# Kernel tuning notes

Measured on AMD Instinct MI355X. Metric: run time of the kernel, lower is better.

The kernel has to match this reference:

```python
import jax, jax.numpy as jnp
import numpy as np

MD = 4  # max displacement -> (2*MD+1)**2 = 81 output channels

def setup_inputs() -> dict:
    key = jax.random.key(0)
    k1, k2 = jax.random.split(key)
    B, C, H, W = 4, 128, 128, 256
    t1 = jax.random.normal(k1, (B, C, H, W), dtype=jnp.float32)
    t2 = jax.random.normal(k2, (B, C, H, W), dtype=jnp.float32)
    return {"t1": t1, "t2": t2}

def reference(t1, t2):
    # PWC-Net correlation: for each displacement (dy,dx) in [-MD,MD]^2,
    # corr[b, d, y, x] = mean_c t1[b,c,y,x] * t2[b,c,y+dy,x+dx]
    B, C, H, W = t1.shape
    t2p = jnp.pad(t2, ((0, 0), (0, 0), (MD, MD), (MD, MD)))
    outs = []
    for dy in range(2 * MD + 1):
        for dx in range(2 * MD + 1):
            shifted = t2p[:, :, dy:dy + H, dx:dx + W]  # (B,C,H,W)
            outs.append(jnp.mean(t1 * shifted, axis=1))  # (B,H,W)
    return jnp.stack(outs, axis=1)  # (B, 81, H, W)
```

## Files before the change

kernel.cpp:

```cpp
#include <hip/hip_runtime.h>

#define MD   4
#define B_   4
#define C_   128
#define H_   128
#define W_   256
#define ND   9
#define NW   9
#define XPT  4

typedef float float4v __attribute__((ext_vector_type(4)));

__global__ __launch_bounds__(NW * 64, 5)
void corr_kernel(const float* __restrict__ t1,
                 const float* __restrict__ t2,
                 float* __restrict__ out) {
    const int tid  = threadIdx.x;
    const int lane = tid & 63;
    const int w    = tid >> 6;
    const int bid  = blockIdx.x;
    const int swz  = (bid & 7) * 64 + (bid >> 3);
    const int y    = swz & (H_ - 1);
    const int b    = swz >> 7;
    const int x0   = lane * XPT;
    const int yy   = y + w - MD;
    const float scale = 1.0f / (float)C_;

    if (yy < 0 || yy >= H_) {
        float4v z = {0.f, 0.f, 0.f, 0.f};
        #pragma unroll
        for (int dx = 0; dx < ND; ++dx) {
            const size_t oidx =
                (((size_t)(b * ND * ND) + w * ND + dx) * H_ + y) * W_ + x0;
            *(float4v*)&out[oidx] = z;
        }
        return;
    }

    float acc[ND][XPT];
    #pragma unroll
    for (int dx = 0; dx < ND; ++dx)
        #pragma unroll
        for (int j = 0; j < XPT; ++j) acc[dx][j] = 0.0f;

    const float* p1 = t1 + (((size_t)(b * C_)) * H_ + y ) * W_ + x0;
    const float* p2 = t2 + (((size_t)(b * C_)) * H_ + yy) * W_ + x0;
    const size_t chstr = (size_t)H_ * W_;

    const bool lm = (lane == 0);
    const bool rm = (lane == 63);

    #pragma unroll 2
    for (int c = 0; c < C_; ++c) {
        const float4v a = *(const float4v*)(p1 + (size_t)c * chstr);
        const float4v v = *(const float4v*)(p2 + (size_t)c * chstr);

        float win[XPT + 2 * MD];
        #pragma unroll
        for (int k = 0; k < 4; ++k) {
            const float up = __shfl_up(v[k], 1);
            const float dn = __shfl_down(v[k], 1);
            win[k]     = lm ? 0.0f : up;
            win[4 + k] = v[k];
            win[8 + k] = rm ? 0.0f : dn;
        }

        #pragma unroll
        for (int dx = 0; dx < ND; ++dx)
            #pragma unroll
            for (int j = 0; j < XPT; ++j)
                acc[dx][j] = fmaf(a[j], win[dx + j], acc[dx][j]);
    }

    #pragma unroll
    for (int dx = 0; dx < ND; ++dx) {
        float4v o;
        #pragma unroll
        for (int j = 0; j < XPT; ++j) o[j] = acc[dx][j] * scale;
        const size_t oidx =
            (((size_t)(b * ND * ND) + w * ND + dx) * H_ + y) * W_ + x0;
        *(float4v*)&out[oidx] = o;
    }
}

extern "C" void kernel_launch(void* const* d_in, const int* in_sizes, int n_in,
                              void* d_out, int out_size, void* d_ws, size_t ws_size,
                              hipStream_t stream) {
    const float* t1 = (const float*)d_in[0];
    const float* t2 = (const float*)d_in[1];
    float* out      = (float*)d_out;
    corr_kernel<<<dim3(B_ * H_), NW * 64, 0, stream>>>(t1, t2, out);
}
```

Measured before the change: 77.21 us.

## Process two output rows per block with eight columns per thread

Each wavefront now splits into two half-waves covering two adjacent output rows, and each thread computes eight x positions instead of four. This halves the grid and gives each thread more FMAs per shuffled neighbour value. Out-of-range rows no longer return early. They clamp their load row and zero the scale factor, so those waves do full, redundant work instead of skipping it. Register pressure rises (72 accumulators) and the occupancy hint drops from 5 to 3.

```diff
diff --git a/kernel.cpp b/kernel.cpp
--- a/kernel.cpp
+++ b/kernel.cpp
@@ -7,11 +7,11 @@
 #define W_   256
 #define ND   9
 #define NW   9
-#define XPT  4
+#define XPT  8
 
 typedef float float4v __attribute__((ext_vector_type(4)));
 
-__global__ __launch_bounds__(NW * 64, 5)
+__global__ __launch_bounds__(NW * 64, 3)
 void corr_kernel(const float* __restrict__ t1,
                  const float* __restrict__ t2,
                  float* __restrict__ out) {
@@ -19,23 +19,20 @@
     const int lane = tid & 63;
     const int w    = tid >> 6;
     const int bid  = blockIdx.x;
-    const int swz  = (bid & 7) * 64 + (bid >> 3);
-    const int y    = swz & (H_ - 1);
-    const int b    = swz >> 7;
-    const int x0   = lane * XPT;
-    const int yy   = y + w - MD;
-    const float scale = 1.0f / (float)C_;
-
-    if (yy < 0 || yy >= H_) {
-        float4v z = {0.f, 0.f, 0.f, 0.f};
-        #pragma unroll
-        for (int dx = 0; dx < ND; ++dx) {
-            const size_t oidx =
-                (((size_t)(b * ND * ND) + w * ND + dx) * H_ + y) * W_ + x0;
-            *(float4v*)&out[oidx] = z;
-        }
-        return;
-    }
+    const int swz  = (bid & 7) * 32 + (bid >> 3);
+    const int yp   = swz & 63;
+    const int b    = swz >> 6;
+    const int y0   = yp * 2;
+    const int half = lane >> 5;
+    const int lx   = lane & 31;
+    const int x0   = lx * XPT;
+    const int yrow = y0 + half;
+    const int yy   = yrow + w - MD;
+    const bool live = (0 <= yy) && (yy < H_);
+    const int  yc  = yy < 0 ? 0 : (yy > H_ - 1 ? H_ - 1 : yy);
+    const float sc = live ? (1.0f / (float)C_) : 0.0f;
+    const bool lm  = (lx == 0);
+    const bool rm  = (lx == 31);
 
     float acc[ND][XPT];
     #pragma unroll
@@ -43,43 +40,48 @@
         #pragma unroll
         for (int j = 0; j < XPT; ++j) acc[dx][j] = 0.0f;
 
-    const float* p1 = t1 + (((size_t)(b * C_)) * H_ + y ) * W_ + x0;
-    const float* p2 = t2 + (((size_t)(b * C_)) * H_ + yy) * W_ + x0;
+    const float* p1 = t1 + (((size_t)(b * C_)) * H_ + yrow) * W_ + x0;
+    const float* p2 = t2 + (((size_t)(b * C_)) * H_ + yc  ) * W_ + x0;
     const size_t chstr = (size_t)H_ * W_;
 
-    const bool lm = (lane == 0);
-    const bool rm = (lane == 63);
-
-    #pragma unroll 2
     for (int c = 0; c < C_; ++c) {
-        const float4v a = *(const float4v*)(p1 + (size_t)c * chstr);
-        const float4v v = *(const float4v*)(p2 + (size_t)c * chstr);
+        const float4v a0 = *(const float4v*)(p1 + (size_t)c * chstr);
+        const float4v a1 = *(const float4v*)(p1 + (size_t)c * chstr + 4);
+        const float4v v0 = *(const float4v*)(p2 + (size_t)c * chstr);
+        const float4v v1 = *(const float4v*)(p2 + (size_t)c * chstr + 4);
 
         float win[XPT + 2 * MD];
         #pragma unroll
         for (int k = 0; k < 4; ++k) {
-            const float up = __shfl_up(v[k], 1);
-            const float dn = __shfl_down(v[k], 1);
-            win[k]     = lm ? 0.0f : up;
-            win[4 + k] = v[k];
-            win[8 + k] = rm ? 0.0f : dn;
+            const float up = __shfl_up(v1[k], 1);
+            const float dn = __shfl_down(v0[k], 1);
+            win[k]      = lm ? 0.0f : up;
+            win[4 + k]  = v0[k];
+            win[8 + k]  = v1[k];
+            win[12 + k] = rm ? 0.0f : dn;
         }
 
         #pragma unroll
         for (int dx = 0; dx < ND; ++dx)
             #pragma unroll
-            for (int j = 0; j < XPT; ++j)
-                acc[dx][j] = fmaf(a[j], win[dx + j], acc[dx][j]);
+            for (int j = 0; j < XPT; ++j) {
+                const float aj = (j < 4) ? a0[j] : a1[j - 4];
+                acc[dx][j] = fmaf(aj, win[dx + j], acc[dx][j]);
+            }
     }
 
     #pragma unroll
     for (int dx = 0; dx < ND; ++dx) {
-        float4v o;
+        float4v o0, o1;
         #pragma unroll
-        for (int j = 0; j < XPT; ++j) o[j] = acc[dx][j] * scale;
+        for (int j = 0; j < 4; ++j) {
+            o0[j] = acc[dx][j]     * sc;
+            o1[j] = acc[dx][4 + j] * sc;
+        }
         const size_t oidx =
-            (((size_t)(b * ND * ND) + w * ND + dx) * H_ + y) * W_ + x0;
-        *(float4v*)&out[oidx] = o;
+            (((size_t)(b * ND * ND) + w * ND + dx) * H_ + yrow) * W_ + x0;
+        *(float4v*)&out[oidx]     = o0;
+        *(float4v*)&out[oidx + 4] = o1;
     }
 }
 
@@ -89,5 +91,5 @@
     const float* t1 = (const float*)d_in[0];
     const float* t2 = (const float*)d_in[1];
     float* out      = (float*)d_out;
-    corr_kernel<<<dim3(B_ * H_), NW * 64, 0, stream>>>(t1, t2, out);
+    corr_kernel<<<dim3(B_ * H_ / 2), NW * 64, 0, stream>>>(t1, t2, out);
 }
```

Result: no change. 77.97 us (+1.0%).

## Split work per (b,y,dy) block with channel halves reduced through LDS

Applied to the files above, without the earlier changes.

Instead of one 9-wave block per output row handling all dy, each block now handles a single (b,y,dy) and uses two waves that each accumulate half the channels, combining partials through shared memory. This gives nine times more, smaller blocks to raise occupancy and balance load, and out-of-range dy blocks write zeros without loading. The cost is losing the sharing of the t1 row across dy waves within a block, so t1 is reloaded by nine blocks and relies on cache reuse via the swizzle, plus an added LDS reduction and barrier.

```diff
diff --git a/kernel.cpp b/kernel.cpp
--- a/kernel.cpp
+++ b/kernel.cpp
@@ -1,41 +1,36 @@
 #include <hip/hip_runtime.h>
 
-#define MD   4
-#define B_   4
-#define C_   128
-#define H_   128
-#define W_   256
-#define ND   9
-#define NW   9
-#define XPT  4
+#define MD    4
+#define B_    4
+#define C_    128
+#define H_    128
+#define W_    256
+#define ND    9
+#define XPT   4
+#define CHALF (C_ / 2)
 
 typedef float float4v __attribute__((ext_vector_type(4)));
 
-__global__ __launch_bounds__(NW * 64, 5)
+__global__ __launch_bounds__(128, 8)
 void corr_kernel(const float* __restrict__ t1,
                  const float* __restrict__ t2,
                  float* __restrict__ out) {
+    __shared__ __align__(16) float pacc[ND][W_];
+
     const int tid  = threadIdx.x;
     const int lane = tid & 63;
-    const int w    = tid >> 6;
+    const int chh  = tid >> 6;
     const int bid  = blockIdx.x;
-    const int swz  = (bid & 7) * 64 + (bid >> 3);
-    const int y    = swz & (H_ - 1);
-    const int b    = swz >> 7;
+    const int swz  = (bid & 7) * 576 + (bid >> 3);
+    const int by   = swz / ND;
+    const int dy   = swz - by * ND;
+    const int b    = by >> 7;
+    const int y    = by & 127;
     const int x0   = lane * XPT;
-    const int yy   = y + w - MD;
-    const float scale = 1.0f / (float)C_;
-
-    if (yy < 0 || yy >= H_) {
-        float4v z = {0.f, 0.f, 0.f, 0.f};
-        #pragma unroll
-        for (int dx = 0; dx < ND; ++dx) {
-            const size_t oidx =
-                (((size_t)(b * ND * ND) + w * ND + dx) * H_ + y) * W_ + x0;
-            *(float4v*)&out[oidx] = z;
-        }
-        return;
-    }
+    const int yy   = y + dy - MD;
+    const bool live = (0 <= yy) && (yy < H_);
+    const bool lm  = (lane == 0);
+    const bool rm  = (lane == 63);
 
     float acc[ND][XPT];
     #pragma unroll
@@ -43,43 +38,59 @@
         #pragma unroll
         for (int j = 0; j < XPT; ++j) acc[dx][j] = 0.0f;
 
-    const float* p1 = t1 + (((size_t)(b * C_)) * H_ + y ) * W_ + x0;
-    const float* p2 = t2 + (((size_t)(b * C_)) * H_ + yy) * W_ + x0;
-    const size_t chstr = (size_t)H_ * W_;
+    if (live) {
+        const float* p1 =
+            t1 + (((size_t)(b * C_ + chh * CHALF)) * H_ + y ) * W_ + x0;
+        const float* p2 =
+            t2 + (((size_t)(b * C_ + chh * CHALF)) * H_ + yy) * W_ + x0;
+        const size_t chstr = (size_t)H_ * W_;
 
-    const bool lm = (lane == 0);
-    const bool rm = (lane == 63);
+        #pragma unroll 2
+        for (int c = 0; c < CHALF; ++c) {
+            const float4v a = *(const float4v*)(p1 + (size_t)c * chstr);
+            const float4v v = *(const float4v*)(p2 + (size_t)c * chstr);
 
-    #pragma unroll 2
-    for (int c = 0; c < C_; ++c) {
-        const float4v a = *(const float4v*)(p1 + (size_t)c * chstr);
-        const float4v v = *(const float4v*)(p2 + (size_t)c * chstr);
+            float win[XPT + 2 * MD];
+            #pragma unroll
+            for (int k = 0; k < 4; ++k) {
+                const float up = __shfl_up(v[k], 1);
+                const float dn = __shfl_down(v[k], 1);
+                win[k]     = lm ? 0.0f : up;
+                win[4 + k] = v[k];
+                win[8 + k] = rm ? 0.0f : dn;
+            }
 
-        float win[XPT + 2 * MD];
+            #pragma unroll
+            for (int dx = 0; dx < ND; ++dx)
+                #pragma unroll
+                for (int j = 0; j < XPT; ++j)
+                    acc[dx][j] = fmaf(a[j], win[dx + j], acc[dx][j]);
+        }
+    }
+
+    if (chh == 0) {
         #pragma unroll
-        for (int k = 0; k < 4; ++k) {
-            const float up = __shfl_up(v[k], 1);
-            const float dn = __shfl_down(v[k], 1);
-            win[k]     = lm ? 0.0f : up;
-            win[4 + k] = v[k];
-            win[8 + k] = rm ? 0.0f : dn;
+        for (int dx = 0; dx < ND; ++dx) {
+            float4v o;
+            #pragma unroll
+            for (int j = 0; j < XPT; ++j) o[j] = acc[dx][j];
+            *(float4v*)&pacc[dx][x0] = o;
         }
-
+    }
+    __syncthreads();
+    if (chh == 1) {
+        const float scale = 1.0f / (float)C_;
         #pragma unroll
-        for (int dx = 0; dx < ND; ++dx)
+        for (int dx = 0; dx < ND; ++dx) {
+            const float4v p = *(const float4v*)&pacc[dx][x0];
+            float4v o;
             #pragma unroll
             for (int j = 0; j < XPT; ++j)
-                acc[dx][j] = fmaf(a[j], win[dx + j], acc[dx][j]);
-    }
-
-    #pragma unroll
-    for (int dx = 0; dx < ND; ++dx) {
-        float4v o;
-        #pragma unroll
-        for (int j = 0; j < XPT; ++j) o[j] = acc[dx][j] * scale;
-        const size_t oidx =
-            (((size_t)(b * ND * ND) + w * ND + dx) * H_ + y) * W_ + x0;
-        *(float4v*)&out[oidx] = o;
+                o[j] = (acc[dx][j] + p[j]) * scale;
+            const size_t oidx =
+                (((size_t)(b * ND * ND) + dy * ND + dx) * H_ + y) * W_ + x0;
+            *(float4v*)&out[oidx] = o;
+        }
     }
 }
 
@@ -89,5 +100,5 @@
     const float* t1 = (const float*)d_in[0];
     const float* t2 = (const float*)d_in[1];
     float* out      = (float*)d_out;
-    corr_kernel<<<dim3(B_ * H_), NW * 64, 0, stream>>>(t1, t2, out);
+    corr_kernel<<<dim3(B_ * H_ * ND), 128, 0, stream>>>(t1, t2, out);
 }
```

New measurement: 105.1 us. +36.2%, slower.

## Retile correlation blocks to 8 rows by 64 columns with two rows per thread

Applied to the files above, without the earlier changes.

Each block now covers an 8-row by 64-column tile rather than a full row. Every thread computes two adjacent output rows, so each t2 row load feeds two accumulator sets. The lane shuffles for neighbour columns are replaced by overlapping vector loads from global memory (left, centre, right), and out-of-range rows are handled by clamping the load and zeroing the scale instead of branching. This aims to improve cache locality and increase work per thread, at the cost of doubled accumulator registers (occupancy hint lowered from 5 to 2) and triple the t2 loads per channel, which must hit in cache.

```diff
diff --git a/kernel.cpp b/kernel.cpp
--- a/kernel.cpp
+++ b/kernel.cpp
@@ -8,10 +8,12 @@
 #define ND   9
 #define NW   9
 #define XPT  4
+#define WQ   64
+#define YB   8
 
 typedef float float4v __attribute__((ext_vector_type(4)));
 
-__global__ __launch_bounds__(NW * 64, 5)
+__global__ __launch_bounds__(NW * 64, 2)
 void corr_kernel(const float* __restrict__ t1,
                  const float* __restrict__ t2,
                  float* __restrict__ out) {
@@ -19,67 +21,87 @@
     const int lane = tid & 63;
     const int w    = tid >> 6;
     const int bid  = blockIdx.x;
-    const int swz  = (bid & 7) * 64 + (bid >> 3);
-    const int y    = swz & (H_ - 1);
-    const int b    = swz >> 7;
-    const int x0   = lane * XPT;
-    const int yy   = y + w - MD;
-    const float scale = 1.0f / (float)C_;
+    const int swz  = (bid & 7) * 32 + (bid >> 3);
+    const int xq   = swz & 3;
+    const int yo   = (swz >> 2) & 15;
+    const int b    = swz >> 6;
+    const int y0   = yo * YB;
+    const int lx   = lane & 15;
+    const int ys   = lane >> 4;
+    const int x0   = xq * WQ + lx * XPT;
+    const int yrA  = y0 + 2 * ys;
+    const int yrB  = yrA + 1;
+    const int yyA  = yrA + w - MD;
+    const int yyB  = yyA + 1;
+    const float scA = (0 <= yyA && yyA < H_) ? (1.0f / (float)C_) : 0.0f;
+    const float scB = (0 <= yyB && yyB < H_) ? (1.0f / (float)C_) : 0.0f;
+    const int ycA  = yyA < 0 ? 0 : (yyA > H_ - 1 ? H_ - 1 : yyA);
+    const int ycB  = yyB < 0 ? 0 : (yyB > H_ - 1 ? H_ - 1 : yyB);
+    const bool lm  = (x0 == 0);
+    const bool rm  = (x0 == W_ - XPT);
+    const int offL = lm ? 0 : -4;
+    const int offR = rm ? 0 :  4;
 
-    if (yy < 0 || yy >= H_) {
-        float4v z = {0.f, 0.f, 0.f, 0.f};
-        #pragma unroll
-        for (int dx = 0; dx < ND; ++dx) {
-            const size_t oidx =
-                (((size_t)(b * ND * ND) + w * ND + dx) * H_ + y) * W_ + x0;
-            *(float4v*)&out[oidx] = z;
-        }
-        return;
-    }
-
-    float acc[ND][XPT];
+    float accA[ND][XPT], accB[ND][XPT];
     #pragma unroll
     for (int dx = 0; dx < ND; ++dx)
         #pragma unroll
-        for (int j = 0; j < XPT; ++j) acc[dx][j] = 0.0f;
+        for (int j = 0; j < XPT; ++j) { accA[dx][j] = 0.0f; accB[dx][j] = 0.0f; }
 
-    const float* p1 = t1 + (((size_t)(b * C_)) * H_ + y ) * W_ + x0;
-    const float* p2 = t2 + (((size_t)(b * C_)) * H_ + yy) * W_ + x0;
     const size_t chstr = (size_t)H_ * W_;
-
-    const bool lm = (lane == 0);
-    const bool rm = (lane == 63);
+    const float* p1A = t1 + (((size_t)(b * C_)) * H_ + yrA) * W_ + x0;
+    const float* p1B = t1 + (((size_t)(b * C_)) * H_ + yrB) * W_ + x0;
+    const float* p2A = t2 + (((size_t)(b * C_)) * H_ + ycA) * W_ + x0;
+    const float* p2B = t2 + (((size_t)(b * C_)) * H_ + ycB) * W_ + x0;
 
     #pragma unroll 2
     for (int c = 0; c < C_; ++c) {
-        const float4v a = *(const float4v*)(p1 + (size_t)c * chstr);
-        const float4v v = *(const float4v*)(p2 + (size_t)c * chstr);
+        const size_t co = (size_t)c * chstr;
+        const float4v aA = *(const float4v*)(p1A + co);
+        const float4v aB = *(const float4v*)(p1B + co);
 
-        float win[XPT + 2 * MD];
+        float4v wlA = *(const float4v*)(p2A + co + offL);
+        const float4v vA = *(const float4v*)(p2A + co);
+        float4v wrA = *(const float4v*)(p2A + co + offR);
+        float4v wlB = *(const float4v*)(p2B + co + offL);
+        const float4v vB = *(const float4v*)(p2B + co);
+        float4v wrB = *(const float4v*)(p2B + co + offR);
+
         #pragma unroll
-        for (int k = 0; k < 4; ++k) {
-            const float up = __shfl_up(v[k], 1);
-            const float dn = __shfl_down(v[k], 1);
-            win[k]     = lm ? 0.0f : up;
-            win[4 + k] = v[k];
-            win[8 + k] = rm ? 0.0f : dn;
+        for (int q = 0; q < 4; ++q) {
+            wlA[q] = lm ? 0.0f : wlA[q];
+            wrA[q] = rm ? 0.0f : wrA[q];
+            wlB[q] = lm ? 0.0f : wlB[q];
+            wrB[q] = rm ? 0.0f : wrB[q];
+        }
+
+        float winA[XPT + 2 * MD], winB[XPT + 2 * MD];
+        #pragma unroll
+        for (int q = 0; q < 4; ++q) {
+            winA[q] = wlA[q]; winA[4 + q] = vA[q]; winA[8 + q] = wrA[q];
+            winB[q] = wlB[q]; winB[4 + q] = vB[q]; winB[8 + q] = wrB[q];
         }
 
         #pragma unroll
         for (int dx = 0; dx < ND; ++dx)
             #pragma unroll
-            for (int j = 0; j < XPT; ++j)
-                acc[dx][j] = fmaf(a[j], win[dx + j], acc[dx][j]);
+            for (int j = 0; j < XPT; ++j) {
+                accA[dx][j] = fmaf(aA[j], winA[dx + j], accA[dx][j]);
+                accB[dx][j] = fmaf(aB[j], winB[dx + j], accB[dx][j]);
+            }
     }
 
     #pragma unroll
     for (int dx = 0; dx < ND; ++dx) {
-        float4v o;
+        float4v oA, oB;
         #pragma unroll
-        for (int j = 0; j < XPT; ++j) o[j] = acc[dx][j] * scale;
-        const size_t oidx =
-            (((size_t)(b * ND * ND) + w * ND + dx) * H_ + y) * W_ + x0;
-        *(float4v*)&out[oidx] = o;
+        for (int j = 0; j < XPT; ++j) {
+            oA[j] = accA[dx][j] * scA;
+            oB[j] = accB[dx][j] * scB;
+        }
+        const size_t pl = (size_t)(b * ND * ND) + w * ND + dx;
+        *(float4v*)&out[(pl * H_ + yrA) * W_ + x0] = oA;
+        *(float4v*)&out[(pl * H_ + yrB) * W_ + x0] = oB;
     }
 }
 
@@ -89,5 +111,5 @@
     const float* t1 = (const float*)d_in[0];
     const float* t2 = (const float*)d_in[1];
     float* out      = (float*)d_out;
-    corr_kernel<<<dim3(B_ * H_), NW * 64, 0, stream>>>(t1, t2, out);
+    corr_kernel<<<dim3(B_ * (H_ / YB) * (W_ / WQ)), NW * 64, 0, stream>>>(t1, t2, out);
 }
```

Measured after the change: 122.6 us. 1.59x slower.
